# Performance work log

Measured on AMD Instinct MI355X. Metric: run time of the kernel, lower is better.

Reference implementation:

```python
import jax, jax.numpy as jnp
import numpy as np

B, N, H, L, K, R = 1024, 64, 128, 4, 16, 20
CUTOFF = 5.0
GAMMA = 10.0   # RBF width
N_TYPES = 10

def _rn(k, shape, scale):
    return jax.random.normal(k, shape, jnp.float32) * scale

def setup_inputs():
    key = jax.random.key(0)
    ks = jax.random.split(key, 16)
    z = lambda *s: jnp.zeros(s, jnp.float32)
    return {
        "positions": _rn(ks[0], (B, N, 3), 2.0),
        "atomic_numbers": jax.random.randint(ks[1], (B, N), 0, N_TYPES),
        "atom_embed": _rn(ks[2], (N_TYPES, H // 4), 0.1),
        "pos_W": _rn(ks[3], (3, 3 * H // 4), 0.5),
        "pos_b": z(3 * H // 4),
        "msg_W": _rn(ks[4], (L, 2 * H + R, H), (2 * H + R) ** -0.5),
        "msg_b": z(L, H),
        "upd_W": _rn(ks[5], (L, H, H), H ** -0.5),
        "upd_b": z(L, H),
        "gself_W": _rn(ks[6], (L, H, H), H ** -0.5),
        "gmean_W": _rn(ks[7], (L, H, H), H ** -0.5),
        "g_b": z(L, H),
        "fus_W": _rn(ks[8], (L, 2 * H, H), (2 * H) ** -0.5),
        "fus_b": z(L, H),
        "ln_g": jnp.ones((L, H), jnp.float32),
        "ln_b": z(L, H),
        "cb_W1": _rn(ks[9], (L, H, 4 * H), H ** -0.5),
        "cb_b1": z(L, 4 * H),
        "cb_W2": _rn(ks[10], (L, 4 * H, H), (4 * H) ** -0.5),
        "cb_b2": z(L, H),
        "fo_W1": _rn(ks[11], (H, H), H ** -0.5),
        "fo_b1": z(H),
        "fo_W2": _rn(ks[12], (H, 3), H ** -0.5),
        "fo_b2": z(3),
    }

def _ln(x, g, b):
    m = x.mean(-1, keepdims=True)
    v = ((x - m) ** 2).mean(-1, keepdims=True)
    return (x - m) * jax.lax.rsqrt(v + 1e-5) * g + b

def reference(positions, atomic_numbers, atom_embed, pos_W, pos_b, msg_W, msg_b,
              upd_W, upd_b, gself_W, gmean_W, g_b, fus_W, fus_b, ln_g, ln_b,
              cb_W1, cb_b1, cb_W2, cb_b2, fo_W1, fo_b1, fo_W2, fo_b2):
    silu = jax.nn.silu
    Bb, Nn, _ = positions.shape
    # embeddings: atom type (H/4) || position (3H/4)
    h = jnp.concatenate([atom_embed[atomic_numbers], positions @ pos_W + pos_b], -1)  # [B,N,H]
    # kNN graph from positions (static across layers since positions are fixed)
    diff = positions[:, :, None, :] - positions[:, None, :, :]
    d2 = jnp.sum(diff * diff, -1) + jnp.eye(Nn, dtype=positions.dtype) * 1e9  # exclude self
    neg_d2, idx = jax.lax.top_k(-d2, K)                       # [B,N,K]
    d = jnp.sqrt(jnp.maximum(-neg_d2, 1e-12))
    centers = jnp.linspace(0.0, CUTOFF, R).astype(positions.dtype)
    rbf = jnp.exp(-GAMMA * (d[..., None] - centers) ** 2)     # [B,N,K,R]
    env = (0.5 * (jnp.cos(jnp.pi * d / CUTOFF) + 1.0) * (d < CUTOFF))[..., None]  # cosine cutoff
    idx_flat = idx.reshape(Bb, Nn * K)
    for i in range(msg_W.shape[0]):
        # local MPNN: gather neighbors, message MLP on [h_i, h_j, rbf], envelope, sum
        h_j = jnp.take_along_axis(h, idx_flat[:, :, None], axis=1).reshape(Bb, Nn, K, -1)
        h_i = jnp.broadcast_to(h[:, :, None, :], h_j.shape)
        m = silu(jnp.concatenate([h_i, h_j, rbf], -1) @ msg_W[i] + msg_b[i]) * env
        local = h + silu(m.sum(2) @ upd_W[i] + upd_b[i])
        # Clifford mean-field: self transform + global-mean transform
        glob = silu(h @ gself_W[i] + h.mean(1, keepdims=True) @ gmean_W[i] + g_b[i])
        # fusion (dropout is identity at inference)
        fused = silu(jnp.concatenate([local, glob], -1) @ fus_W[i] + fus_b[i])
        # Clifford block: pre-LN residual MLP
        x = _ln(fused, ln_g[i], ln_b[i])
        h = fused + silu(x @ cb_W1[i] + cb_b1[i]) @ cb_W2[i] + cb_b2[i]
    return silu(h @ fo_W1 + fo_b1) @ fo_W2 + fo_b2  # [B,N,3] forces
```

## Files before the change

### kernel.cpp

```cpp
#include <hip/hip_runtime.h>

typedef unsigned short ushort_t;
typedef unsigned int uint_t;
typedef unsigned long long ull_t;
typedef __attribute__((ext_vector_type(8))) short short8;
typedef __attribute__((ext_vector_type(4))) float f32x4;

#define B_ 1024
#define N_ 64
#define H_ 128
#define NT 256

#define IMG_WI 0
#define IMG_WJ 16384
#define IMG_UW 32768
#define IMG_GS 49152
#define IMG_FT 65536
#define IMG_FB 81920
#define IMG_C1 98304
#define IMG_C2 163840
#define IMG_GMT 229376
#define IMG_RW 245760
#define IMG_L 249856
#define IMG_FO 999424

__device__ __forceinline__ ushort_t f2bf(float f) {
    return __builtin_bit_cast(ushort_t, (__bf16)f);
}
__device__ __forceinline__ float bf2f(ushort_t u) {
    union { uint_t i; float f; } v; v.i = ((uint_t)u) << 16; return v.f;
}
__device__ __forceinline__ float siluf(float x) { return x / (1.0f + __expf(-x)); }

__device__ __forceinline__ int sidx(int m, int k) {
    return m * H_ + (((k >> 3) ^ (m & 7)) << 3) + (k & 7);
}
__device__ __forceinline__ int fragoff(int m, int ch) {
    return m * H_ + ((ch ^ (m & 7)) << 3);
}

extern "C" __global__ __launch_bounds__(256)
void convert_weights(const float* __restrict__ msg_W, const float* __restrict__ upd_W,
                     const float* __restrict__ gself_W, const float* __restrict__ fus_W,
                     const float* __restrict__ cb_W1, const float* __restrict__ cb_W2,
                     const float* __restrict__ gmean_W, const float* __restrict__ fo_W1,
                     ushort_t* __restrict__ wimg)
{
    __shared__ ushort_t tile[128][34];
    const int g = blockIdx.x;
    const int tid = threadIdx.x;
    const float* W; int ld = 128, k0 = 0, c0; ushort_t* dst;
    if (g >= 244) {
        int st = g - 244;
        W = fo_W1; c0 = st * 32; dst = wimg + IMG_FO + st * 4096;
    } else {
        const int l = g / 61, r = g - l * 61;
        ushort_t* base = wimg + l * IMG_L;
        if (r == 60) {
            const float* Wr = msg_W + l * 35328 + 256 * 128;
            ushort_t* drw = base + IMG_RW;
            for (int e = 0; e < 16; ++e) {
                int q = threadIdx.x * 16 + e;
                int sub = q >> 10, n = (q >> 5) & 31, k = q & 31;
                drw[q] = f2bf(k < 20 ? Wr[(size_t)k * 128 + sub * 32 + n] : 0.0f);
            }
            return;
        }
        int off, st;
        if      (r < 4)  { W = msg_W + l * 35328;            st = r;      off = IMG_WI;  c0 = st * 32; }
        else if (r < 8)  { W = msg_W + l * 35328;  k0 = 128; st = r - 4;  off = IMG_WJ;  c0 = st * 32; }
        else if (r < 12) { W = upd_W + l * 16384;            st = r - 8;  off = IMG_UW;  c0 = st * 32; }
        else if (r < 16) { W = gself_W + l * 16384;          st = r - 12; off = IMG_GS;  c0 = st * 32; }
        else if (r < 20) { W = fus_W + l * 32768;            st = r - 16; off = IMG_FT;  c0 = st * 32; }
        else if (r < 24) { W = fus_W + l * 32768;  k0 = 128; st = r - 20; off = IMG_FB;  c0 = st * 32; }
        else if (r < 40) { W = cb_W1 + l * 65536;  ld = 512; st = r - 24; off = IMG_C1;  c0 = st * 32; }
        else if (r < 56) { int j = (r - 40) >> 2; W = cb_W2 + l * 65536; k0 = j * 128;
                           st = r - 40; off = IMG_C2; c0 = ((r - 40) & 3) * 32; }
        else             { W = gmean_W + l * 16384;          st = r - 56; off = IMG_GMT; c0 = st * 32; }
        dst = base + off + st * 4096;
    }
    const int kr = tid >> 5, n = tid & 31;
    #pragma unroll
    for (int p = 0; p < 16; ++p) {
        int k = p * 8 + kr;
        tile[k][n] = f2bf(W[(size_t)(k0 + k) * ld + c0 + n]);
    }
    __syncthreads();
    {
        int n2 = tid >> 3, kk = (tid & 7) << 4;
        short8 v0, v1;
        #pragma unroll
        for (int e = 0; e < 8; ++e) v0[e] = (short)tile[kk + e][n2];
        #pragma unroll
        for (int e = 0; e < 8; ++e) v1[e] = (short)tile[kk + 8 + e][n2];
        *(short8*)(dst + n2 * 128 + kk) = v0;
        *(short8*)(dst + n2 * 128 + kk + 8) = v1;
    }
}

struct __align__(16) Smem {
    ushort_t T1[N_ * H_];
    ushort_t T2[N_ * H_];
    ushort_t T3[N_ * H_];
    float d[1024];
    float env[1024];
    ushort_t idx[1024];
    char u[2048];
};

__device__ __forceinline__ f32x4 gemm_s(const short8 a[4], const ushort_t* __restrict__ img,
                                        int s, int l15, int quad)
{
    const ushort_t* base = img + ((s >> 1) << 12) + ((((s & 1) << 4) + l15) << 7) + quad * 8;
    short8 b0 = *(const short8*)(base);
    short8 b1 = *(const short8*)(base + 32);
    short8 b2 = *(const short8*)(base + 64);
    short8 b3 = *(const short8*)(base + 96);
    f32x4 c = {0.f, 0.f, 0.f, 0.f};
    c = __builtin_amdgcn_mfma_f32_16x16x32_bf16(a[0], b0, c, 0, 0, 0);
    c = __builtin_amdgcn_mfma_f32_16x16x32_bf16(a[1], b1, c, 0, 0, 0);
    c = __builtin_amdgcn_mfma_f32_16x16x32_bf16(a[2], b2, c, 0, 0, 0);
    c = __builtin_amdgcn_mfma_f32_16x16x32_bf16(a[3], b3, c, 0, 0, 0);
    return c;
}
__device__ __forceinline__ f32x4 gemm_s_acc(const short8 a[4], const ushort_t* __restrict__ img,
                                            int s, int l15, int quad, f32x4 c)
{
    const ushort_t* base = img + ((s >> 1) << 12) + ((((s & 1) << 4) + l15) << 7) + quad * 8;
    short8 b0 = *(const short8*)(base);
    short8 b1 = *(const short8*)(base + 32);
    short8 b2 = *(const short8*)(base + 64);
    short8 b3 = *(const short8*)(base + 96);
    c = __builtin_amdgcn_mfma_f32_16x16x32_bf16(a[0], b0, c, 0, 0, 0);
    c = __builtin_amdgcn_mfma_f32_16x16x32_bf16(a[1], b1, c, 0, 0, 0);
    c = __builtin_amdgcn_mfma_f32_16x16x32_bf16(a[2], b2, c, 0, 0, 0);
    c = __builtin_amdgcn_mfma_f32_16x16x32_bf16(a[3], b3, c, 0, 0, 0);
    return c;
}
__device__ __forceinline__ void loadA(const ushort_t* __restrict__ X, int mrow, int quad, short8 a[4]) {
    #pragma unroll
    for (int kc = 0; kc < 4; ++kc) a[kc] = *(const short8*)&X[fragoff(mrow, kc * 4 + quad)];
}

extern "C" __global__ __launch_bounds__(NT, 2)
void md17_fused_kernel(
    const float* __restrict__ positions, const int* __restrict__ atomic_numbers,
    const float* __restrict__ atom_embed, const float* __restrict__ pos_W,
    const float* __restrict__ pos_b,
    const float* __restrict__ msg_b, const float* __restrict__ upd_b,
    const float* __restrict__ g_b, const float* __restrict__ fus_b,
    const float* __restrict__ ln_g, const float* __restrict__ ln_b,
    const float* __restrict__ cb_b1, const float* __restrict__ cb_b2,
    const float* __restrict__ fo_b1,
    const float* __restrict__ fo_W2, const float* __restrict__ fo_b2,
    char* __restrict__ ws, float* __restrict__ out)
{
    __shared__ Smem sm;
    const int b = blockIdx.x;
    const int tid = threadIdx.x;
    const int wave = tid >> 6, lane = tid & 63;
    const int quad = lane >> 4, l15 = lane & 15;
    const int mrow = wave * 16 + l15;
    const int rbase = wave * 16 + quad * 4;

    const ushort_t* wimg = (const ushort_t*)ws;
    float* spos = (float*)sm.u;
    ushort_t* part = (ushort_t*)sm.u;
    float* hmean = (float*)(sm.u + 1024);
    float* gvec  = (float*)(sm.u + 1536);

    float hreg[8][4];

    if (tid < 192) spos[tid] = positions[b * 192 + tid];
    __syncthreads();

    {
        float cx[4], cy[4], cz[4];
        #pragma unroll
        for (int j = 0; j < 4; ++j) {
            cx[j] = spos[(l15 * 4 + j) * 3 + 0];
            cy[j] = spos[(l15 * 4 + j) * 3 + 1];
            cz[j] = spos[(l15 * 4 + j) * 3 + 2];
        }
        #pragma unroll 1
        for (int it = 0; it < 4; ++it) {
            const int n = wave * 16 + it * 4 + quad;
            float nx = spos[n * 3 + 0], ny = spos[n * 3 + 1], nz = spos[n * 3 + 2];
            float d2[4];
            #pragma unroll
            for (int j = 0; j < 4; ++j) {
                float dx = __fsub_rn(nx, cx[j]);
                float dy = __fsub_rn(ny, cy[j]);
                float dz = __fsub_rn(nz, cz[j]);
                d2[j] = __fadd_rn(__fadd_rn(__fmul_rn(dx, dx), __fmul_rn(dy, dy)),
                                  __fmul_rn(dz, dz));
                if (l15 * 4 + j == n) d2[j] = 1e30f;
            }
            #pragma unroll 1
            for (int k = 0; k < 16; ++k) {
                float lm = d2[0];
                if (d2[1] < lm) lm = d2[1];
                if (d2[2] < lm) lm = d2[2];
                if (d2[3] < lm) lm = d2[3];
                float gm = lm;
                #pragma unroll
                for (int o = 1; o < 16; o <<= 1) gm = fminf(gm, __shfl_xor(gm, o));
                ull_t bal = __ballot(lm == gm);
                int wl = __ffsll((bal >> (quad * 16)) & 0xFFFFull) - 1;
                if (l15 == wl) {
                    int jstar = 3;
                    if (d2[2] == gm) jstar = 2;
                    if (d2[1] == gm) jstar = 1;
                    if (d2[0] == gm) jstar = 0;
                    #pragma unroll
                    for (int j = 0; j < 4; ++j) if (j == jstar) d2[j] = 1e30f;
                    float dd = sqrtf(fmaxf(gm, 1e-12f));
                    sm.d[n * 16 + k] = dd;
                    sm.env[n * 16 + k] = (dd < 5.0f)
                        ? 0.5f * (__cosf(0.62831853071795864769f * dd) + 1.0f) : 0.0f;
                    sm.idx[n * 16 + k] = (ushort_t)(wl * 4 + jstar);
                }
            }
        }
    }

    {
        int an[4];
        #pragma unroll
        for (int r = 0; r < 4; ++r) an[r] = atomic_numbers[b * N_ + rbase + r];
        #pragma unroll
        for (int s = 0; s < 8; ++s) {
            int col = s * 16 + l15;
            #pragma unroll
            for (int r = 0; r < 4; ++r) {
                float v;
                if (s < 2) {
                    v = atom_embed[an[r] * 32 + col];
                } else {
                    int j = col - 32;
                    v = pos_b[j];
                    #pragma unroll
                    for (int c = 0; c < 3; ++c)
                        v = fmaf(spos[(rbase + r) * 3 + c], pos_W[c * 96 + j], v);
                }
                hreg[s][r] = v;
                sm.T3[sidx(rbase + r, col)] = f2bf(v);
            }
        }
    }
    __syncthreads();
    #pragma unroll
    for (int s = 0; s < 8; ++s) {
        int col = s * 16 + l15;
        float p = hreg[s][0] + hreg[s][1] + hreg[s][2] + hreg[s][3];
        p += __shfl_xor(p, 16);
        p += __shfl_xor(p, 32);
        if (quad == 0) part[wave * 128 + col] = f2bf(p);
    }

    #pragma unroll 1
    for (int l = 0; l < 4; ++l) {
        const ushort_t* wl = wimg + l * IMG_L;
        const float* mb  = msg_b + l * H_;
        const float* ub  = upd_b + l * H_;
        const float* gb  = g_b + l * H_;
        const float* fb  = fus_b + l * H_;
        const float* lg  = ln_g + l * H_;
        const float* lb  = ln_b + l * H_;
        const float* c1b = cb_b1 + l * 4 * H_;
        const float* c2b = cb_b2 + l * H_;

        __syncthreads();
        if (tid < H_)
            hmean[tid] = (bf2f(part[tid]) + bf2f(part[128 + tid])
                        + bf2f(part[256 + tid]) + bf2f(part[384 + tid])) * (1.0f / 64.0f);
        __syncthreads();

        if (tid < H_) {
            float s = gb[tid];
            const ushort_t* wrow = wl + IMG_GMT + tid * 128;
            for (int c = 0; c < 128; c += 8) {
                short8 w = *(const short8*)(wrow + c);
                #pragma unroll
                for (int i = 0; i < 8; ++i) s = fmaf(hmean[c + i], bf2f((ushort_t)w[i]), s);
            }
            gvec[tid] = s;
        }
        {
            short8 a_h[4]; loadA(sm.T3, mrow, quad, a_h);
            #pragma unroll 2
            for (int s = 0; s < 8; ++s) {
                f32x4 c = gemm_s(a_h, wl + IMG_WI, s, l15, quad);
                int col = s * 16 + l15; float bv = mb[col];
                #pragma unroll
                for (int r = 0; r < 4; ++r)
                    sm.T1[sidx(rbase + r, col)] = f2bf(c[r] + bv);
            }
            #pragma unroll 2
            for (int s = 0; s < 8; ++s) {
                f32x4 c = gemm_s(a_h, wl + IMG_WJ, s, l15, quad);
                int col = s * 16 + l15;
                #pragma unroll
                for (int r = 0; r < 4; ++r)
                    sm.T2[sidx(rbase + r, col)] = f2bf(c[r]);
            }
        }
        __syncthreads();

        {
            float ccv[8];
            #pragma unroll
            for (int j = 0; j < 8; ++j)
                ccv[j] = (float)((double)(quad * 8 + j) * (5.0 / 19.0));
            #pragma unroll 1
            for (int g = 0; g < 16; ++g) {
                int n = wave * 16 + g;
                int jv[4]; float ev[4];
                #pragma unroll
                for (int r = 0; r < 4; ++r) {
                    int k = quad * 4 + r;
                    jv[r] = sm.idx[n * 16 + k];
                    ev[r] = sm.env[n * 16 + k];
                }
                float ddm = sm.d[n * 16 + l15];
                short8 arb;
                #pragma unroll
                for (int j = 0; j < 8; ++j) {
                    float t2 = ddm - ccv[j];
                    float rv = __expf(-10.0f * t2 * t2);
                    arb[j] = (short)((quad * 8 + j) < 20 ? f2bf(rv) : (ushort_t)0);
                }
                #pragma unroll
                for (int s = 0; s < 8; ++s) {
                    int col = s * 16 + l15;
                    const ushort_t* rbase_p = wl + IMG_RW + ((s >> 1) << 10)
                                            + ((((s & 1) << 4) + l15) << 5) + quad * 8;
                    short8 brw = *(const short8*)rbase_p;
                    f32x4 c = {0.f, 0.f, 0.f, 0.f};
                    c = __builtin_amdgcn_mfma_f32_16x16x32_bf16(arb, brw, c, 0, 0, 0);
                    float ai = bf2f(sm.T1[sidx(n, col)]);
                    float acc = 0.f;
                    #pragma unroll
                    for (int r = 0; r < 4; ++r) {
                        float gm = bf2f(sm.T2[sidx(jv[r], col)]);
                        acc = fmaf(siluf(ai + gm + c[r]), ev[r], acc);
                    }
                    acc += __shfl_xor(acc, 16);
                    acc += __shfl_xor(acc, 32);
                    if (quad == 0) sm.T1[sidx(n, col)] = f2bf(acc);
                }
            }
        }
        __syncthreads();


        {
            short8 a_m[4]; loadA(sm.T1, mrow, quad, a_m);
            #pragma unroll
            for (int s = 0; s < 8; ++s) {
                f32x4 c = gemm_s(a_m, wl + IMG_UW, s, l15, quad);
                int col = s * 16 + l15; float bv = ub[col];
                #pragma unroll
                for (int r = 0; r < 4; ++r)
                    sm.T2[sidx(rbase + r, col)] = f2bf(hreg[s][r] + siluf(c[r] + bv));
            }
            short8 a_h[4]; loadA(sm.T3, mrow, quad, a_h);
            #pragma unroll 2
            for (int s = 0; s < 8; ++s) {
                f32x4 c = gemm_s(a_h, wl + IMG_GS, s, l15, quad);
                int col = s * 16 + l15; float gv = gvec[col];
                #pragma unroll
                for (int r = 0; r < 4; ++r)
                    sm.T1[sidx(rbase + r, col)] = f2bf(siluf(c[r] + gv));
            }
        }

        float sr[4] = {0.f, 0.f, 0.f, 0.f}, qr[4] = {0.f, 0.f, 0.f, 0.f};
        {
            short8 a_t[4];
            loadA(sm.T2, mrow, quad, a_t);
            #pragma unroll
            for (int s = 0; s < 8; ++s) {
                f32x4 c = gemm_s(a_t, wl + IMG_FT, s, l15, quad);
                #pragma unroll
                for (int r = 0; r < 4; ++r) hreg[s][r] = c[r];
            }
            loadA(sm.T1, mrow, quad, a_t);
            #pragma unroll
            for (int s = 0; s < 8; ++s) {
                f32x4 c = gemm_s(a_t, wl + IMG_FB, s, l15, quad);
                int col = s * 16 + l15; float bv = fb[col];
                #pragma unroll
                for (int r = 0; r < 4; ++r) {
                    float v = siluf(hreg[s][r] + c[r] + bv);
                    hreg[s][r] = v;
                    sr[r] += v; qr[r] += v * v;
                }
            }
            #pragma unroll
            for (int o = 1; o < 16; o <<= 1) {
                #pragma unroll
                for (int r = 0; r < 4; ++r) {
                    sr[r] += __shfl_xor(sr[r], o);
                    qr[r] += __shfl_xor(qr[r], o);
                }
            }
        }

        #pragma unroll
        for (int r = 0; r < 4; ++r) {
            float mu = sr[r] * (1.0f / 128.0f);
            float var = qr[r] * (1.0f / 128.0f) - mu * mu;
            float rs = rsqrtf(var + 1e-5f);
            int row = rbase + r;
            #pragma unroll
            for (int s = 0; s < 8; ++s) {
                int col = s * 16 + l15;
                sm.T1[sidx(row, col)] = f2bf((hreg[s][r] - mu) * rs * lg[col] + lb[col]);
            }
        }

        {
            f32x4 acc2[8];
            #pragma unroll
            for (int s = 0; s < 8; ++s) {
                int col = s * 16 + l15; float bv = c2b[col];
                #pragma unroll
                for (int r = 0; r < 4; ++r) acc2[s][r] = hreg[s][r] + bv;
            }
            #pragma unroll 1
            for (int j = 0; j < 4; ++j) {
                short8 a_x[4]; loadA(sm.T1, mrow, quad, a_x);
                #pragma unroll 2
                for (int s = 0; s < 8; ++s) {
                    f32x4 c = gemm_s(a_x, wl + IMG_C1 + j * 16384, s, l15, quad);
                    int col = s * 16 + l15; float bv = c1b[j * H_ + col];
                    #pragma unroll
                    for (int r = 0; r < 4; ++r)
                        sm.T2[sidx(rbase + r, col)] = f2bf(siluf(c[r] + bv));
                }
                short8 a_t[4]; loadA(sm.T2, mrow, quad, a_t);
                #pragma unroll
                for (int s = 0; s < 8; ++s)
                    acc2[s] = gemm_s_acc(a_t, wl + IMG_C2 + j * 16384, s, l15, quad, acc2[s]);
            }
            #pragma unroll
            for (int s = 0; s < 8; ++s) {
                int col = s * 16 + l15;
                float p = 0.f;
                #pragma unroll
                for (int r = 0; r < 4; ++r) {
                    float v = acc2[s][r];
                    hreg[s][r] = v;
                    sm.T3[sidx(rbase + r, col)] = f2bf(v);
                    p += v;
                }
                p += __shfl_xor(p, 16);
                p += __shfl_xor(p, 32);
                if (quad == 0) part[wave * 128 + col] = f2bf(p);
            }
        }
    }

    {
        short8 a_f[4]; loadA(sm.T3, mrow, quad, a_f);
        #pragma unroll 2
        for (int s = 0; s < 8; ++s) {
            f32x4 c = gemm_s(a_f, wimg + IMG_FO, s, l15, quad);
            int col = s * 16 + l15; float bv = fo_b1[col];
            #pragma unroll
            for (int r = 0; r < 4; ++r)
                sm.T2[sidx(rbase + r, col)] = f2bf(siluf(c[r] + bv));
        }
    }
    __syncthreads();
    if (tid < 192) {
        int n = tid / 3, j = tid - n * 3;
        float s = fo_b2[j];
        #pragma unroll 1
        for (int ch = 0; ch < 16; ++ch) {
            short8 v = *(const short8*)&sm.T2[fragoff(n, ch)];
            #pragma unroll
            for (int i = 0; i < 8; ++i)
                s = fmaf(bf2f((ushort_t)v[i]), fo_W2[(ch * 8 + i) * 3 + j], s);
        }
        out[b * 192 + tid] = s;
    }
}

extern "C" void kernel_launch(void* const* d_in, const int* in_sizes, int n_in,
                              void* d_out, int out_size, void* d_ws, size_t ws_size,
                              hipStream_t stream) {
    (void)in_sizes; (void)n_in; (void)out_size; (void)ws_size;
    convert_weights<<<248, 256, 0, stream>>>(
        (const float*)d_in[5], (const float*)d_in[7], (const float*)d_in[9],
        (const float*)d_in[12], (const float*)d_in[16], (const float*)d_in[18],
        (const float*)d_in[10], (const float*)d_in[20], (ushort_t*)d_ws);
    md17_fused_kernel<<<B_, NT, 0, stream>>>(
        (const float*)d_in[0], (const int*)d_in[1],
        (const float*)d_in[2], (const float*)d_in[3], (const float*)d_in[4],
        (const float*)d_in[6], (const float*)d_in[8],
        (const float*)d_in[11], (const float*)d_in[13],
        (const float*)d_in[14], (const float*)d_in[15],
        (const float*)d_in[17], (const float*)d_in[19],
        (const float*)d_in[21],
        (const float*)d_in[22], (const float*)d_in[23],
        (char*)d_ws, (float*)d_out);
}
```

Before: 1.204 ms.

## Compute global-mean transform via MFMA on h then reduce, removing per-layer barriers

Uses linearity, mean(h) @ W equals mean(h @ W), to drop the separate hmean reduction and the scalar 128x128 matvec. Each layer now runs one extra MFMA GEMM of h against the gmean weights and reduces its rows into fp32 partials. This removes two __syncthreads per layer and a serial matvec done by half the threads, and the per-row sums are no longer rounded to bf16. The cost is a full 64x128x128 MFMA GEMM per layer, and two loops are also unrolled by 2.

Result: slower. 1.268 ms (+5.4%).

```diff
diff --git a/kernel.cpp b/kernel.cpp
--- a/kernel.cpp
+++ b/kernel.cpp
@@ -105,7 +105,7 @@
     float d[1024];
     float env[1024];
     ushort_t idx[1024];
-    char u[2048];
+    char u[2560];
 };
 
 __device__ __forceinline__ f32x4 gemm_s(const short8 a[4], const ushort_t* __restrict__ img,
@@ -164,10 +164,9 @@
     const int rbase = wave * 16 + quad * 4;
 
     const ushort_t* wimg = (const ushort_t*)ws;
-    float* spos = (float*)sm.u;
-    ushort_t* part = (ushort_t*)sm.u;
-    float* hmean = (float*)(sm.u + 1024);
-    float* gvec  = (float*)(sm.u + 1536);
+    float* spos  = (float*)sm.u;
+    float* part2 = (float*)sm.u;
+    float* gvec  = (float*)(sm.u + 2048);
 
     float hreg[8][4];
 
@@ -249,14 +248,6 @@
         }
     }
     __syncthreads();
-    #pragma unroll
-    for (int s = 0; s < 8; ++s) {
-        int col = s * 16 + l15;
-        float p = hreg[s][0] + hreg[s][1] + hreg[s][2] + hreg[s][3];
-        p += __shfl_xor(p, 16);
-        p += __shfl_xor(p, 32);
-        if (quad == 0) part[wave * 128 + col] = f2bf(p);
-    }
 
     #pragma unroll 1
     for (int l = 0; l < 4; ++l) {
@@ -270,22 +261,6 @@
         const float* c1b = cb_b1 + l * 4 * H_;
         const float* c2b = cb_b2 + l * H_;
 
-        __syncthreads();
-        if (tid < H_)
-            hmean[tid] = (bf2f(part[tid]) + bf2f(part[128 + tid])
-                        + bf2f(part[256 + tid]) + bf2f(part[384 + tid])) * (1.0f / 64.0f);
-        __syncthreads();
-
-        if (tid < H_) {
-            float s = gb[tid];
-            const ushort_t* wrow = wl + IMG_GMT + tid * 128;
-            for (int c = 0; c < 128; c += 8) {
-                short8 w = *(const short8*)(wrow + c);
-                #pragma unroll
-                for (int i = 0; i < 8; ++i) s = fmaf(hmean[c + i], bf2f((ushort_t)w[i]), s);
-            }
-            gvec[tid] = s;
-        }
         {
             short8 a_h[4]; loadA(sm.T3, mrow, quad, a_h);
             #pragma unroll 2
@@ -304,15 +279,27 @@
                 for (int r = 0; r < 4; ++r)
                     sm.T2[sidx(rbase + r, col)] = f2bf(c[r]);
             }
+            #pragma unroll 2
+            for (int s = 0; s < 8; ++s) {
+                f32x4 c = gemm_s(a_h, wl + IMG_GMT, s, l15, quad);
+                float p = c[0] + c[1] + c[2] + c[3];
+                p += __shfl_xor(p, 16);
+                p += __shfl_xor(p, 32);
+                if (quad == 0) part2[wave * 128 + s * 16 + l15] = p;
+            }
         }
         __syncthreads();
+
+        if (tid < H_)
+            gvec[tid] = (part2[tid] + part2[128 + tid] + part2[256 + tid]
+                       + part2[384 + tid]) * (1.0f / 64.0f) + gb[tid];
 
         {
             float ccv[8];
             #pragma unroll
             for (int j = 0; j < 8; ++j)
                 ccv[j] = (float)((double)(quad * 8 + j) * (5.0 / 19.0));
-            #pragma unroll 1
+            #pragma unroll 2
             for (int g = 0; g < 16; ++g) {
                 int n = wave * 16 + g;
                 int jv[4]; float ev[4];
@@ -428,7 +415,7 @@
                 #pragma unroll
                 for (int r = 0; r < 4; ++r) acc2[s][r] = hreg[s][r] + bv;
             }
-            #pragma unroll 1
+            #pragma unroll 2
             for (int j = 0; j < 4; ++j) {
                 short8 a_x[4]; loadA(sm.T1, mrow, quad, a_x);
                 #pragma unroll 2
@@ -447,17 +434,12 @@
             #pragma unroll
             for (int s = 0; s < 8; ++s) {
                 int col = s * 16 + l15;
-                float p = 0.f;
                 #pragma unroll
                 for (int r = 0; r < 4; ++r) {
                     float v = acc2[s][r];
                     hreg[s][r] = v;
                     sm.T3[sidx(rbase + r, col)] = f2bf(v);
-                    p += v;
-                }
-                p += __shfl_xor(p, 16);
-                p += __shfl_xor(p, 32);
-                if (quad == 0) part[wave * 128 + col] = f2bf(p);
+                }
             }
         }
     }
```
